# Performance work log

Hardware: AMD Instinct MI355X
Metric: run time of the kernel (lower is better)

Reference implementation:

```python
import jax, jax.numpy as jnp
import numpy as np

B, S, DIM, H, C = 1, 1024, 4096, 32, 8
HD = DIM // H  # 128
NEG = -1e9


def setup_inputs() -> dict:
    key = jax.random.key(0)
    ks = jax.random.split(key, 8)
    scale = 0.02
    x = jax.random.normal(ks[0], (B, S, DIM), jnp.float32)
    wq = jax.random.normal(ks[1], (DIM, DIM), jnp.float32) * scale
    wk = jax.random.normal(ks[2], (DIM, DIM), jnp.float32) * scale
    wv = jax.random.normal(ks[3], (DIM, DIM), jnp.float32) * scale
    wo = jax.random.normal(ks[4], (DIM, DIM), jnp.float32) * scale
    # RoPE tables (theta=10000), matching precompute_freqs_cis
    inv = 1.0 / (10000.0 ** (np.arange(0, HD, 2, dtype=np.float32) / HD))  # [HD/2]
    ang = np.arange(S, dtype=np.float32)[:, None] * inv[None, :]  # [S, HD/2]
    freqs_cos = jnp.asarray(np.cos(ang))
    freqs_sin = jnp.asarray(np.sin(ang))
    # causal mask used at prefill (start_pos == 0)
    mask = jnp.where(jnp.triu(jnp.ones((S, S), bool), k=1), jnp.float32(NEG), 0.0)
    # cluster labels: ensure every cluster non-empty; rep = first head with label
    rng = np.random.default_rng(0)
    lab = np.concatenate([np.arange(C), rng.integers(0, C, H - C)]).astype(np.int32)
    rep = np.array([np.where(lab == c)[0][0] for c in range(C)], dtype=np.int32)
    return {
        "x": x, "wq": wq, "wk": wk, "wv": wv, "wo": wo,
        "freqs_cos": freqs_cos, "freqs_sin": freqs_sin, "mask": mask,
        "cluster_assignment": jnp.asarray(lab), "rep_heads": jnp.asarray(rep),
        "start_pos": 0,
    }


def _rope(x, cos, sin):
    # x: [b, s, h, d]; cos/sin: [s, d/2]; interleaved complex multiply
    xr, xi = x[..., ::2], x[..., 1::2]
    cos = cos[None, :, None, :]
    sin = sin[None, :, None, :]
    orr = xr * cos - xi * sin
    oi = xr * sin + xi * cos
    return jnp.stack([orr, oi], axis=-1).reshape(x.shape)


def reference(x, wq, wk, wv, wo, freqs_cos, freqs_sin, mask,
              cluster_assignment, rep_heads, start_pos):
    b, s, dim = x.shape
    h, d = H, HD
    xq = (x @ wq.T).reshape(b, s, h, d)
    xk = (x @ wk.T).reshape(b, s, h, d)
    xv = (x @ wv.T).reshape(b, s, h, d)
    xq = _rope(xq, freqs_cos, freqs_sin)
    xk = _rope(xk, freqs_cos, freqs_sin)
    xqh = jnp.transpose(xq, (0, 2, 1, 3))  # [b, h, s, d]
    xkh = jnp.transpose(xk, (0, 2, 1, 3))
    vh = jnp.transpose(xv, (0, 2, 1, 3))
    # CHAI: gather representative head per cluster, score once per cluster
    xq_new = xqh[:, rep_heads]  # [b, C, s, d]
    xk_new = xkh[:, rep_heads]
    sc = jnp.einsum("bcqd,bckd->bcqk", xq_new, xk_new) / jnp.sqrt(jnp.float32(d))
    # scatter cluster scores back to every member head (pure gather by label)
    scores = sc[:, cluster_assignment]  # [b, h, s, s]
    scores = scores + mask[None, None]
    p = jax.nn.softmax(scores.astype(jnp.float32), axis=-1).astype(x.dtype)
    out = jnp.einsum("bhqk,bhkd->bhqd", p, vh)
    out = jnp.transpose(out, (0, 2, 1, 3)).reshape(b, s, h * d)
    return out @ wo.T
```

## Files before the change

kernel.cpp:

```cpp
#include <hip/hip_runtime.h>

typedef __bf16 bf16x8 __attribute__((ext_vector_type(8)));
typedef float f32x4 __attribute__((ext_vector_type(4)));
typedef unsigned short u16x8 __attribute__((ext_vector_type(8)));

#define BM 128
#define BN 128
#define BK 64

__device__ __forceinline__ unsigned short f2bf(float f) {
    union { float f; unsigned int u; } x; x.f = f;
    unsigned int u = x.u;
    u += 0x7fffu + ((u >> 16) & 1u);
    return (unsigned short)(u >> 16);
}

__device__ __forceinline__ float bf2f(unsigned short h) {
    union { unsigned int u; float f; } x; x.u = ((unsigned int)h) << 16;
    return x.f;
}

__device__ __forceinline__ void async_copy16(const void* g, void* l) {
    __builtin_amdgcn_global_load_lds(
        (const __attribute__((address_space(1))) void*)(uintptr_t)g,
        (__attribute__((address_space(3))) void*)(uintptr_t)l, 16, 0, 0);
}

__global__ void cvt_all(const float* __restrict__ x, const float* __restrict__ wq,
                        const float* __restrict__ wk, const float* __restrict__ wv,
                        const float* __restrict__ wo, const int* __restrict__ rep,
                        unsigned short* __restrict__ xb, unsigned short* __restrict__ wqkvb,
                        unsigned short* __restrict__ wob) {
    long i = (long)blockIdx.x * 256 + threadIdx.x;
    const float* src;
    unsigned short* dst;
    if (i < 524288) {
        src = x + i * 8;
        dst = xb + i * 8;
    } else if (i < 3670016) {
        long j = i - 524288;
        int r = (int)(j >> 9), c8 = (int)(j & 511);
        const float* s;
        if (r < 1024)      s = wq + ((long)(rep[r >> 7] * 128 + (r & 127)) << 12);
        else if (r < 2048) s = wk + ((long)(rep[(r - 1024) >> 7] * 128 + (r & 127)) << 12);
        else               s = wv + ((long)(r - 2048) << 12);
        src = s + c8 * 8;
        dst = wqkvb + ((long)r << 12) + c8 * 8;
    } else {
        long j = i - 3670016;
        src = wo + j * 8;
        dst = wob + j * 8;
    }
    float4 v0 = ((const float4*)src)[0];
    float4 v1 = ((const float4*)src)[1];
    u16x8 o = { f2bf(v0.x), f2bf(v0.y), f2bf(v0.z), f2bf(v0.w),
                f2bf(v1.x), f2bf(v1.y), f2bf(v1.z), f2bf(v1.w) };
    *(u16x8*)dst = o;
}


template<bool F32OUT, int MODE>
__global__ __launch_bounds__(256, 2) void gemm_bt(
    const unsigned short* __restrict__ A, const unsigned short* __restrict__ B,
    void* __restrict__ Cv, int K, int lda, int ldb, int ldc,
    long long aZ, long long bZ, long long cZ, const int* __restrict__ aIdx,
    int kOffZ, int nby) {
    __shared__ unsigned short As[BM * BK];
    __shared__ unsigned short Bs[BN * BK];

    int L = blockIdx.x;
    int q8 = gridDim.x >> 3;
    int wk_ = (L & 7) * q8 + (L >> 3);
    int bmi = wk_ & 7;
    int t2 = wk_ >> 3;
    int bni = t2 % nby;
    int z = t2 / nby;

    if (MODE == 1 && bni > bmi) return;

    A += (aIdx ? (long long)aIdx[z] : (long long)z) * aZ;
    B += (long long)z * bZ;
    int bm = bmi * BM;
    int bn = bni * BN;
    int t = threadIdx.x;
    int lane = t & 63;
    int w = t >> 6;
    int wr = (w >> 1) * 64, wc = (w & 1) * 64;

    int kt0 = z * kOffZ;
    int kEnd = kt0 + K;
    if (MODE == 2) kEnd = kt0 + min(K, bm + BM);

    f32x4 acc[4][4] = {};

    for (int kt = kt0; kt < kEnd; kt += BK) {
#pragma unroll
        for (int i = 0; i < 4; ++i) {
            int f = i * 256 + t;
            int row = f >> 3;
            int c8 = f & 7;
            async_copy16(A + (long)(bm + row) * lda + kt + c8 * 8, &As[f * 8]);
            async_copy16(B + (long)(bn + row) * ldb + kt + c8 * 8, &Bs[f * 8]);
        }
        asm volatile("s_waitcnt vmcnt(0)" ::: "memory");
        __syncthreads();
#pragma unroll
        for (int kk = 0; kk < BK; kk += 32) {
            bf16x8 a[4], b[4];
            int r0 = lane & 15;
            int kof = kk + ((lane >> 4) << 3);
#pragma unroll
            for (int m = 0; m < 4; ++m)
                a[m] = *(const bf16x8*)&As[(wr + m * 16 + r0) * BK + kof];
#pragma unroll
            for (int n = 0; n < 4; ++n)
                b[n] = *(const bf16x8*)&Bs[(wc + n * 16 + r0) * BK + kof];
#pragma unroll
            for (int m = 0; m < 4; ++m)
#pragma unroll
                for (int n = 0; n < 4; ++n)
                    acc[m][n] = __builtin_amdgcn_mfma_f32_16x16x32_bf16(a[m], b[n], acc[m][n], 0, 0, 0);
        }
        __syncthreads();
    }

    int cl = lane & 15;
    int rbase = (lane >> 4) << 2;
    if (F32OUT) {
        float* C = (float*)Cv + (long long)z * cZ;
#pragma unroll
        for (int m = 0; m < 4; ++m)
#pragma unroll
            for (int n = 0; n < 4; ++n)
#pragma unroll
                for (int j = 0; j < 4; ++j)
                    C[(long)(bm + wr + m * 16 + rbase + j) * ldc + (bn + wc + n * 16 + cl)] = acc[m][n][j];
    } else {
        unsigned short* C = (unsigned short*)Cv + (long long)z * cZ;
#pragma unroll
        for (int m = 0; m < 4; ++m)
#pragma unroll
            for (int n = 0; n < 4; ++n)
#pragma unroll
                for (int j = 0; j < 4; ++j)
                    C[(long)(bm + wr + m * 16 + rbase + j) * ldc + (bn + wc + n * 16 + cl)] = f2bf(acc[m][n][j]);
    }
}

__global__ void reduce_rope(unsigned short* __restrict__ qkv,
                            const float* __restrict__ fc, const float* __restrict__ fs,
                            int nsplit) {
    int s = blockIdx.y;
    int cc = (blockIdx.x * 256 + threadIdx.x) * 8;
    long base = (long)s * 6144 + cc;
    ushort4 a0 = *(const ushort4*)(qkv + base);
    ushort4 a1 = *(const ushort4*)(qkv + base + 4);
    float f[8] = { bf2f(a0.x), bf2f(a0.y), bf2f(a0.z), bf2f(a0.w),
                   bf2f(a1.x), bf2f(a1.y), bf2f(a1.z), bf2f(a1.w) };
    for (int z = 1; z < nsplit; ++z) {
        const unsigned short* p = qkv + (long)z * 6291456;
        ushort4 b0 = *(const ushort4*)(p + base);
        ushort4 b1 = *(const ushort4*)(p + base + 4);
        f[0] += bf2f(b0.x); f[1] += bf2f(b0.y); f[2] += bf2f(b0.z); f[3] += bf2f(b0.w);
        f[4] += bf2f(b1.x); f[5] += bf2f(b1.y); f[6] += bf2f(b1.z); f[7] += bf2f(b1.w);
    }
    if (cc < 2048) {
        int i0 = (cc & 127) >> 1;
        const float* cp = fc + (s << 6) + i0;
        const float* sp = fs + (s << 6) + i0;
#pragma unroll
        for (int p = 0; p < 4; ++p) {
            float co = cp[p], sn = sp[p];
            float x0 = f[2 * p], x1 = f[2 * p + 1];
            f[2 * p] = x0 * co - x1 * sn;
            f[2 * p + 1] = x0 * sn + x1 * co;
        }
    }
    ushort4 o0 = { f2bf(f[0]), f2bf(f[1]), f2bf(f[2]), f2bf(f[3]) };
    ushort4 o1 = { f2bf(f[4]), f2bf(f[5]), f2bf(f[6]), f2bf(f[7]) };
    *(ushort4*)(qkv + base) = o0;
    *(ushort4*)(qkv + base + 4) = o1;
}

__global__ void reduce_out4(const unsigned short* __restrict__ p, float* __restrict__ out) {
    long i = (long)blockIdx.x * 256 + threadIdx.x;
    ushort4 a = ((const ushort4*)p)[i];
    ushort4 b = ((const ushort4*)(p + 4194304))[i];
    ushort4 c = ((const ushort4*)(p + 8388608))[i];
    ushort4 d = ((const ushort4*)(p + 12582912))[i];
    float4 o;
    o.x = bf2f(a.x) + bf2f(b.x) + bf2f(c.x) + bf2f(d.x);
    o.y = bf2f(a.y) + bf2f(b.y) + bf2f(c.y) + bf2f(d.y);
    o.z = bf2f(a.z) + bf2f(b.z) + bf2f(c.z) + bf2f(d.z);
    o.w = bf2f(a.w) + bf2f(b.w) + bf2f(c.w) + bf2f(d.w);
    ((float4*)out)[i] = o;
}

__global__ void transpose_v(const unsigned short* __restrict__ qkv, unsigned short* __restrict__ vt) {
    __shared__ unsigned short tile[32][33];
    int h = blockIdx.z, d0 = blockIdx.x * 32, s0 = blockIdx.y * 32;
    int tx = threadIdx.x & 31, ty = threadIdx.x >> 5;
#pragma unroll
    for (int i = 0; i < 32; i += 8)
        tile[ty + i][tx] = qkv[(long)(s0 + ty + i) * 6144 + 2048 + h * 128 + d0 + tx];
    __syncthreads();
#pragma unroll
    for (int i = 0; i < 32; i += 8)
        vt[(long)h * 131072 + (long)(d0 + ty + i) * 1024 + s0 + tx] = tile[tx][ty + i];
}

__global__ __launch_bounds__(256) void softmax_causal(const unsigned short* __restrict__ sc,
                                                      unsigned short* __restrict__ P) {
    int i = blockIdx.x;
    int c = blockIdx.y;
    long base = ((long)c << 20) + ((long)i << 10);
    const unsigned short* row = sc + base;
    unsigned short* prow = P + base;
    int t = threadIdx.x;
    const float alpha = 0.08838834764831845f;
    int nj = i >> 8;

    float v[4];
    float mx = -3.4e38f;
    for (int j0 = 0; j0 <= nj; ++j0) {
        int j = j0 * 256 + t;
        float x = bf2f(row[j]) * alpha;
        v[j0] = (j <= i) ? x : -3.4e38f;
        mx = fmaxf(mx, v[j0]);
    }
#pragma unroll
    for (int o = 32; o > 0; o >>= 1) mx = fmaxf(mx, __shfl_xor(mx, o));
    __shared__ float red[4];
    int w = t >> 6, lane = t & 63;
    if (lane == 0) red[w] = mx;
    __syncthreads();
    mx = fmaxf(fmaxf(red[0], red[1]), fmaxf(red[2], red[3]));

    float e[4];
    float sum = 0.f;
    for (int j0 = 0; j0 <= nj; ++j0) {
        e[j0] = (v[j0] > -1e37f) ? __expf(v[j0] - mx) : 0.f;
        sum += e[j0];
    }
#pragma unroll
    for (int o = 32; o > 0; o >>= 1) sum += __shfl_xor(sum, o);
    __syncthreads();
    if (lane == 0) red[w] = sum;
    __syncthreads();
    sum = red[0] + red[1] + red[2] + red[3];
    float inv = 1.f / sum;
    for (int j0 = 0; j0 <= nj; ++j0) {
        int j = j0 * 256 + t;
        prow[j] = f2bf(e[j0] * inv);
    }
}


extern "C" void kernel_launch(void* const* d_in, const int* in_sizes, int n_in,
                              void* d_out, int out_size, void* d_ws, size_t ws_size,
                              hipStream_t stream) {
    const float* x  = (const float*)d_in[0];
    const float* wq = (const float*)d_in[1];
    const float* wk = (const float*)d_in[2];
    const float* wv = (const float*)d_in[3];
    const float* wo = (const float*)d_in[4];
    const float* fc = (const float*)d_in[5];
    const float* fs = (const float*)d_in[6];
    const int* lab = (const int*)d_in[8];
    const int* rep = (const int*)d_in[9];
    float* out = (float*)d_out;

    char* ws = (char*)d_ws;
    unsigned short* xb    = (unsigned short*)(ws);
    unsigned short* wqkvb = (unsigned short*)(ws + 8388608);
    unsigned short* wob   = (unsigned short*)(ws + 58720256);
    unsigned short* qkv_s = (unsigned short*)(ws + 92274688);
    unsigned short* vt    = (unsigned short*)(ws + 104857600);
    unsigned short* scores= (unsigned short*)(ws + 8388608);
    unsigned short* P     = (unsigned short*)(ws + 41943040);
    unsigned short* opart = (unsigned short*)(ws + 8388608);
    unsigned short* attn  = xb;

    int skQ = (ws_size >= (size_t)117440512) ? 2 : 1;

    cvt_all<<<22528, 256, 0, stream>>>(x, wq, wk, wv, wo, rep, xb, wqkvb, wob);

    if (skQ == 2) {
        gemm_bt<false, 0><<<768, 256, 0, stream>>>(
            xb, wqkvb, qkv_s, 2048, 4096, 4096, 6144, 0, 0, 6291456, nullptr, 2048, 48);
    } else {
        gemm_bt<false, 0><<<384, 256, 0, stream>>>(
            xb, wqkvb, qkv_s, 4096, 4096, 4096, 6144, 0, 0, 0, nullptr, 0, 48);
    }

    reduce_rope<<<dim3(3, 1024), 256, 0, stream>>>(qkv_s, fc, fs, skQ);
    transpose_v<<<dim3(4, 32, 32), 256, 0, stream>>>(qkv_s, vt);

    gemm_bt<false, 1><<<512, 256, 0, stream>>>(
        qkv_s, qkv_s + 1024, scores, 128, 6144, 6144, 1024,
        128, 128, 1048576, nullptr, 0, 8);

    softmax_causal<<<dim3(1024, 8), 256, 0, stream>>>(scores, P);

    gemm_bt<false, 2><<<256, 256, 0, stream>>>(
        P, vt, attn, 1024, 1024, 1024, 4096,
        1048576, 131072, 128, lab, 0, 1);

    gemm_bt<false, 0><<<1024, 256, 0, stream>>>(
        attn, wob, opart, 1024, 4096, 4096, 4096, 0, 0, 4194304, nullptr, 1024, 32);
    reduce_out4<<<4096, 256, 0, stream>>>(opart, out);
}
```

Measured before the change: 218.2 us.

## Fuse fp32 weight conversion into GEMM loads and swizzle LDS tiles

Removes the separate pass that converted all four fp32 weight matrices to bf16. The QKV and output-projection GEMMs now stream fp32 weights straight into LDS, convert them to bf16 in registers before the MFMA, and apply the representative-head gather inside the kernel. All GEMMs also gain an XOR-swizzled LDS layout to cut bank conflicts. The trade is twice the weight bytes per tile and a larger LDS footprint (fp32 B tile), which may lower occupancy.

New measurement: 211.3 us. 1.03x faster.

```diff
diff --git a/kernel.cpp b/kernel.cpp
--- a/kernel.cpp
+++ b/kernel.cpp
@@ -26,45 +26,118 @@
         (__attribute__((address_space(3))) void*)(uintptr_t)l, 16, 0, 0);
 }
 
-__global__ void cvt_all(const float* __restrict__ x, const float* __restrict__ wq,
-                        const float* __restrict__ wk, const float* __restrict__ wv,
-                        const float* __restrict__ wo, const int* __restrict__ rep,
-                        unsigned short* __restrict__ xb, unsigned short* __restrict__ wqkvb,
-                        unsigned short* __restrict__ wob) {
+__global__ void cvt_x(const float* __restrict__ x, unsigned short* __restrict__ xb) {
     long i = (long)blockIdx.x * 256 + threadIdx.x;
-    const float* src;
-    unsigned short* dst;
-    if (i < 524288) {
-        src = x + i * 8;
-        dst = xb + i * 8;
-    } else if (i < 3670016) {
-        long j = i - 524288;
-        int r = (int)(j >> 9), c8 = (int)(j & 511);
-        const float* s;
-        if (r < 1024)      s = wq + ((long)(rep[r >> 7] * 128 + (r & 127)) << 12);
-        else if (r < 2048) s = wk + ((long)(rep[(r - 1024) >> 7] * 128 + (r & 127)) << 12);
-        else               s = wv + ((long)(r - 2048) << 12);
-        src = s + c8 * 8;
-        dst = wqkvb + ((long)r << 12) + c8 * 8;
-    } else {
-        long j = i - 3670016;
-        src = wo + j * 8;
-        dst = wob + j * 8;
-    }
+    const float* src = x + i * 8;
     float4 v0 = ((const float4*)src)[0];
     float4 v1 = ((const float4*)src)[1];
     u16x8 o = { f2bf(v0.x), f2bf(v0.y), f2bf(v0.z), f2bf(v0.w),
                 f2bf(v1.x), f2bf(v1.y), f2bf(v1.z), f2bf(v1.w) };
-    *(u16x8*)dst = o;
-}
-
-
-template<bool F32OUT, int MODE>
+    *(u16x8*)(xb + i * 8) = o;
+}
+
+template<int GATHER>
+__global__ __launch_bounds__(256, 2) void gemm_wf32(
+    const unsigned short* __restrict__ A, const float* __restrict__ w0,
+    const float* __restrict__ w1, const float* __restrict__ w2,
+    const int* __restrict__ rep, unsigned short* __restrict__ C,
+    int K, int lda, int ldc, long long cZ, int kOffZ, int nby) {
+    __shared__ unsigned short As[BM * BK];
+    __shared__ float BsF[BN * BK];
+
+    int L = blockIdx.x;
+    int q8 = gridDim.x >> 3;
+    int wk_ = (L & 7) * q8 + (L >> 3);
+    int bmi = wk_ & 7;
+    int t2 = wk_ >> 3;
+    int bni = t2 % nby;
+    int z = t2 / nby;
+
+    const float* Bsrc;
+    if (GATHER) {
+        if (bni < 8)       Bsrc = w0 + (long)rep[bni] * 524288;
+        else if (bni < 16) Bsrc = w1 + (long)rep[bni - 8] * 524288;
+        else               Bsrc = w2 + (long)(bni - 16) * 524288;
+    } else {
+        Bsrc = w0 + (long)bni * 524288;
+    }
+
+    int bm = bmi * BM;
+    int t = threadIdx.x;
+    int lane = t & 63;
+    int w = t >> 6;
+    int wr = (w >> 1) * 64, wc = (w & 1) * 64;
+
+    int kt0 = z * kOffZ;
+    int kEnd = kt0 + K;
+
+    f32x4 acc[4][4] = {};
+
+    for (int kt = kt0; kt < kEnd; kt += BK) {
+#pragma unroll
+        for (int i = 0; i < 4; ++i) {
+            int f = i * 256 + t;
+            int row = f >> 3, c8 = f & 7;
+            int cs = c8 ^ (row & 7);
+            async_copy16(A + (long)(bm + row) * lda + kt + cs * 8, &As[f * 8]);
+        }
+#pragma unroll
+        for (int i = 0; i < 8; ++i) {
+            int f = i * 256 + t;
+            int row = f >> 4, c16 = f & 15;
+            int pair = c16 >> 1, w2b = c16 & 1;
+            int ps = pair ^ (row & 7);
+            async_copy16(Bsrc + (long)row * 4096 + kt + ps * 8 + w2b * 4, &BsF[f * 4]);
+        }
+        asm volatile("s_waitcnt vmcnt(0)" ::: "memory");
+        __syncthreads();
+#pragma unroll
+        for (int kk = 0; kk < BK; kk += 32) {
+            bf16x8 a[4], b[4];
+            int r0 = lane & 15;
+            int kof = kk + ((lane >> 4) << 3);
+            int kc = kof >> 3;
+#pragma unroll
+            for (int m = 0; m < 4; ++m) {
+                int ra = wr + m * 16 + r0;
+                a[m] = *(const bf16x8*)&As[ra * 64 + ((kc ^ (ra & 7)) << 3)];
+            }
+#pragma unroll
+            for (int n = 0; n < 4; ++n) {
+                int rb = wc + n * 16 + r0;
+                const f32x4* pb = (const f32x4*)&BsF[rb * 64 + ((kc ^ (rb & 7)) << 3)];
+                f32x4 lo = pb[0], hi = pb[1];
+                bf16x8 bb = { (__bf16)lo[0], (__bf16)lo[1], (__bf16)lo[2], (__bf16)lo[3],
+                              (__bf16)hi[0], (__bf16)hi[1], (__bf16)hi[2], (__bf16)hi[3] };
+                b[n] = bb;
+            }
+#pragma unroll
+            for (int m = 0; m < 4; ++m)
+#pragma unroll
+                for (int n = 0; n < 4; ++n)
+                    acc[m][n] = __builtin_amdgcn_mfma_f32_16x16x32_bf16(a[m], b[n], acc[m][n], 0, 0, 0);
+        }
+        __syncthreads();
+    }
+
+    int cl = lane & 15;
+    int rbase = (lane >> 4) << 2;
+    unsigned short* Cp = C + (long long)z * cZ;
+#pragma unroll
+    for (int m = 0; m < 4; ++m)
+#pragma unroll
+        for (int n = 0; n < 4; ++n)
+#pragma unroll
+            for (int j = 0; j < 4; ++j)
+                Cp[(long)(bm + wr + m * 16 + rbase + j) * ldc + (bni * BN + wc + n * 16 + cl)] = f2bf(acc[m][n][j]);
+}
+
+template<int MODE>
 __global__ __launch_bounds__(256, 2) void gemm_bt(
     const unsigned short* __restrict__ A, const unsigned short* __restrict__ B,
-    void* __restrict__ Cv, int K, int lda, int ldb, int ldc,
+    unsigned short* __restrict__ C, int K, int lda, int ldb, int ldc,
     long long aZ, long long bZ, long long cZ, const int* __restrict__ aIdx,
-    int kOffZ, int nby) {
+    int nby) {
     __shared__ unsigned short As[BM * BK];
     __shared__ unsigned short Bs[BN * BK];
 
@@ -87,20 +160,18 @@
     int w = t >> 6;
     int wr = (w >> 1) * 64, wc = (w & 1) * 64;
 
-    int kt0 = z * kOffZ;
-    int kEnd = kt0 + K;
-    if (MODE == 2) kEnd = kt0 + min(K, bm + BM);
+    int kEnd = (MODE == 2) ? min(K, bm + BM) : K;
 
     f32x4 acc[4][4] = {};
 
-    for (int kt = kt0; kt < kEnd; kt += BK) {
+    for (int kt = 0; kt < kEnd; kt += BK) {
 #pragma unroll
         for (int i = 0; i < 4; ++i) {
             int f = i * 256 + t;
-            int row = f >> 3;
-            int c8 = f & 7;
-            async_copy16(A + (long)(bm + row) * lda + kt + c8 * 8, &As[f * 8]);
-            async_copy16(B + (long)(bn + row) * ldb + kt + c8 * 8, &Bs[f * 8]);
+            int row = f >> 3, c8 = f & 7;
+            int cs = c8 ^ (row & 7);
+            async_copy16(A + (long)(bm + row) * lda + kt + cs * 8, &As[f * 8]);
+            async_copy16(B + (long)(bn + row) * ldb + kt + cs * 8, &Bs[f * 8]);
         }
         asm volatile("s_waitcnt vmcnt(0)" ::: "memory");
         __syncthreads();
@@ -109,12 +180,17 @@
             bf16x8 a[4], b[4];
             int r0 = lane & 15;
             int kof = kk + ((lane >> 4) << 3);
-#pragma unroll
-            for (int m = 0; m < 4; ++m)
-                a[m] = *(const bf16x8*)&As[(wr + m * 16 + r0) * BK + kof];
-#pragma unroll
-            for (int n = 0; n < 4; ++n)
-                b[n] = *(const bf16x8*)&Bs[(wc + n * 16 + r0) * BK + kof];
+            int kc = kof >> 3;
+#pragma unroll
+            for (int m = 0; m < 4; ++m) {
+                int ra = wr + m * 16 + r0;
+                a[m] = *(const bf16x8*)&As[ra * 64 + ((kc ^ (ra & 7)) << 3)];
+            }
+#pragma unroll
+            for (int n = 0; n < 4; ++n) {
+                int rb = wc + n * 16 + r0;
+                b[n] = *(const bf16x8*)&Bs[rb * 64 + ((kc ^ (rb & 7)) << 3)];
+            }
 #pragma unroll
             for (int m = 0; m < 4; ++m)
 #pragma unroll
@@ -126,25 +202,14 @@
 
     int cl = lane & 15;
     int rbase = (lane >> 4) << 2;
-    if (F32OUT) {
-        float* C = (float*)Cv + (long long)z * cZ;
-#pragma unroll
-        for (int m = 0; m < 4; ++m)
-#pragma unroll
-            for (int n = 0; n < 4; ++n)
-#pragma unroll
-                for (int j = 0; j < 4; ++j)
-                    C[(long)(bm + wr + m * 16 + rbase + j) * ldc + (bn + wc + n * 16 + cl)] = acc[m][n][j];
-    } else {
-        unsigned short* C = (unsigned short*)Cv + (long long)z * cZ;
-#pragma unroll
-        for (int m = 0; m < 4; ++m)
-#pragma unroll
-            for (int n = 0; n < 4; ++n)
-#pragma unroll
-                for (int j = 0; j < 4; ++j)
-                    C[(long)(bm + wr + m * 16 + rbase + j) * ldc + (bn + wc + n * 16 + cl)] = f2bf(acc[m][n][j]);
-    }
+    unsigned short* Cp = C + (long long)z * cZ;
+#pragma unroll
+    for (int m = 0; m < 4; ++m)
+#pragma unroll
+        for (int n = 0; n < 4; ++n)
+#pragma unroll
+            for (int j = 0; j < 4; ++j)
+                Cp[(long)(bm + wr + m * 16 + rbase + j) * ldc + (bn + wc + n * 16 + cl)] = f2bf(acc[m][n][j]);
 }
 
 __global__ void reduce_rope(unsigned short* __restrict__ qkv,
@@ -272,41 +337,39 @@
 
     char* ws = (char*)d_ws;
     unsigned short* xb    = (unsigned short*)(ws);
-    unsigned short* wqkvb = (unsigned short*)(ws + 8388608);
-    unsigned short* wob   = (unsigned short*)(ws + 58720256);
-    unsigned short* qkv_s = (unsigned short*)(ws + 92274688);
-    unsigned short* vt    = (unsigned short*)(ws + 104857600);
     unsigned short* scores= (unsigned short*)(ws + 8388608);
     unsigned short* P     = (unsigned short*)(ws + 41943040);
     unsigned short* opart = (unsigned short*)(ws + 8388608);
+    unsigned short* qkv_s = (unsigned short*)(ws + 92274688);
+    unsigned short* vt    = (unsigned short*)(ws + 104857600);
     unsigned short* attn  = xb;
 
     int skQ = (ws_size >= (size_t)117440512) ? 2 : 1;
 
-    cvt_all<<<22528, 256, 0, stream>>>(x, wq, wk, wv, wo, rep, xb, wqkvb, wob);
+    cvt_x<<<2048, 256, 0, stream>>>(x, xb);
 
     if (skQ == 2) {
-        gemm_bt<false, 0><<<768, 256, 0, stream>>>(
-            xb, wqkvb, qkv_s, 2048, 4096, 4096, 6144, 0, 0, 6291456, nullptr, 2048, 48);
+        gemm_wf32<1><<<768, 256, 0, stream>>>(
+            xb, wq, wk, wv, rep, qkv_s, 2048, 4096, 6144, 6291456, 2048, 48);
     } else {
-        gemm_bt<false, 0><<<384, 256, 0, stream>>>(
-            xb, wqkvb, qkv_s, 4096, 4096, 4096, 6144, 0, 0, 0, nullptr, 0, 48);
+        gemm_wf32<1><<<384, 256, 0, stream>>>(
+            xb, wq, wk, wv, rep, qkv_s, 4096, 4096, 6144, 0, 0, 48);
     }
 
     reduce_rope<<<dim3(3, 1024), 256, 0, stream>>>(qkv_s, fc, fs, skQ);
     transpose_v<<<dim3(4, 32, 32), 256, 0, stream>>>(qkv_s, vt);
 
-    gemm_bt<false, 1><<<512, 256, 0, stream>>>(
+    gemm_bt<1><<<512, 256, 0, stream>>>(
         qkv_s, qkv_s + 1024, scores, 128, 6144, 6144, 1024,
-        128, 128, 1048576, nullptr, 0, 8);
+        128, 128, 1048576, nullptr, 8);
 
     softmax_causal<<<dim3(1024, 8), 256, 0, stream>>>(scores, P);
 
-    gemm_bt<false, 2><<<256, 256, 0, stream>>>(
+    gemm_bt<2><<<256, 256, 0, stream>>>(
         P, vt, attn, 1024, 1024, 1024, 4096,
-        1048576, 131072, 128, lab, 0, 1);
-
-    gemm_bt<false, 0><<<1024, 256, 0, stream>>>(
-        attn, wob, opart, 1024, 4096, 4096, 4096, 0, 0, 4194304, nullptr, 1024, 32);
+        1048576, 131072, 128, lab, 1);
+
+    gemm_wf32<0><<<1024, 256, 0, stream>>>(
+        attn, wo, nullptr, nullptr, nullptr, opart, 1024, 4096, 4096, 4194304, 1024, 32);
     reduce_out4<<<4096, 256, 0, stream>>>(opart, out);
 }
```

## Double-buffer LDS tiles and XOR-swizzle columns in bf16 GEMM kernel

Applied to the files above, without the earlier changes.

The shared GEMM kernel now keeps two LDS buffers per operand, so the async global-to-LDS copy of the next K tile is issued before the MFMA work on the current tile. The global wait and barrier move to the end of each iteration. The 16-byte chunk index within each 128-byte LDS row is XOR-swizzled by the row index on both store and load, to cut bank conflicts on the row-strided fragment reads. The unused float-output template path is dropped. LDS per block doubles to 64KB, which may limit occupancy under the two-blocks-per-CU launch bound.

Result: faster. 203.9 us (-6.6%).

```diff
diff --git a/kernel.cpp b/kernel.cpp
--- a/kernel.cpp
+++ b/kernel.cpp
@@ -58,15 +58,14 @@
     *(u16x8*)dst = o;
 }
 
-
-template<bool F32OUT, int MODE>
+template<int MODE>
 __global__ __launch_bounds__(256, 2) void gemm_bt(
     const unsigned short* __restrict__ A, const unsigned short* __restrict__ B,
-    void* __restrict__ Cv, int K, int lda, int ldb, int ldc,
+    unsigned short* __restrict__ C, int K, int lda, int ldb, int ldc,
     long long aZ, long long bZ, long long cZ, const int* __restrict__ aIdx,
     int kOffZ, int nby) {
-    __shared__ unsigned short As[BM * BK];
-    __shared__ unsigned short Bs[BN * BK];
+    __shared__ unsigned short As[2][BM * BK];
+    __shared__ unsigned short Bs[2][BN * BK];
 
     int L = blockIdx.x;
     int q8 = gridDim.x >> 3;
@@ -87,64 +86,69 @@
     int w = t >> 6;
     int wr = (w >> 1) * 64, wc = (w & 1) * 64;
 
-    int kt0 = z * kOffZ;
-    int kEnd = kt0 + K;
-    if (MODE == 2) kEnd = kt0 + min(K, bm + BM);
+    int kt0 = (MODE == 0) ? z * kOffZ : 0;
+    int kEnd = kt0 + ((MODE == 2) ? min(K, bm + BM) : K);
+
+#define STAGE(buf, kt) \
+    _Pragma("unroll") \
+    for (int i = 0; i < 4; ++i) { \
+        int f = i * 256 + t; \
+        int row = f >> 3, c8 = f & 7; \
+        int cs = c8 ^ (row & 7); \
+        async_copy16(A + (long)(bm + row) * lda + (kt) + cs * 8, &As[buf][f * 8]); \
+        async_copy16(B + (long)(bn + row) * ldb + (kt) + cs * 8, &Bs[buf][f * 8]); \
+    }
 
     f32x4 acc[4][4] = {};
 
+    STAGE(0, kt0);
+    asm volatile("s_waitcnt vmcnt(0)" ::: "memory");
+    __syncthreads();
+
+    int cur = 0;
     for (int kt = kt0; kt < kEnd; kt += BK) {
-#pragma unroll
-        for (int i = 0; i < 4; ++i) {
-            int f = i * 256 + t;
-            int row = f >> 3;
-            int c8 = f & 7;
-            async_copy16(A + (long)(bm + row) * lda + kt + c8 * 8, &As[f * 8]);
-            async_copy16(B + (long)(bn + row) * ldb + kt + c8 * 8, &Bs[f * 8]);
-        }
-        asm volatile("s_waitcnt vmcnt(0)" ::: "memory");
-        __syncthreads();
+        if (kt + BK < kEnd) { STAGE(cur ^ 1, kt + BK); }
+
+        const unsigned short* Asc = As[cur];
+        const unsigned short* Bsc = Bs[cur];
 #pragma unroll
         for (int kk = 0; kk < BK; kk += 32) {
             bf16x8 a[4], b[4];
             int r0 = lane & 15;
             int kof = kk + ((lane >> 4) << 3);
-#pragma unroll
-            for (int m = 0; m < 4; ++m)
-                a[m] = *(const bf16x8*)&As[(wr + m * 16 + r0) * BK + kof];
-#pragma unroll
-            for (int n = 0; n < 4; ++n)
-                b[n] = *(const bf16x8*)&Bs[(wc + n * 16 + r0) * BK + kof];
+            int kc = kof >> 3;
+#pragma unroll
+            for (int m = 0; m < 4; ++m) {
+                int ra = wr + m * 16 + r0;
+                a[m] = *(const bf16x8*)&Asc[ra * 64 + ((kc ^ (ra & 7)) << 3)];
+            }
+#pragma unroll
+            for (int n = 0; n < 4; ++n) {
+                int rb = wc + n * 16 + r0;
+                b[n] = *(const bf16x8*)&Bsc[rb * 64 + ((kc ^ (rb & 7)) << 3)];
+            }
 #pragma unroll
             for (int m = 0; m < 4; ++m)
 #pragma unroll
                 for (int n = 0; n < 4; ++n)
                     acc[m][n] = __builtin_amdgcn_mfma_f32_16x16x32_bf16(a[m], b[n], acc[m][n], 0, 0, 0);
         }
+        asm volatile("s_waitcnt vmcnt(0)" ::: "memory");
         __syncthreads();
-    }
+        cur ^= 1;
+    }
+#undef STAGE
 
     int cl = lane & 15;
     int rbase = (lane >> 4) << 2;
-    if (F32OUT) {
-        float* C = (float*)Cv + (long long)z * cZ;
-#pragma unroll
-        for (int m = 0; m < 4; ++m)
-#pragma unroll
-            for (int n = 0; n < 4; ++n)
-#pragma unroll
-                for (int j = 0; j < 4; ++j)
-                    C[(long)(bm + wr + m * 16 + rbase + j) * ldc + (bn + wc + n * 16 + cl)] = acc[m][n][j];
-    } else {
-        unsigned short* C = (unsigned short*)Cv + (long long)z * cZ;
-#pragma unroll
-        for (int m = 0; m < 4; ++m)
-#pragma unroll
-            for (int n = 0; n < 4; ++n)
-#pragma unroll
-                for (int j = 0; j < 4; ++j)
-                    C[(long)(bm + wr + m * 16 + rbase + j) * ldc + (bn + wc + n * 16 + cl)] = f2bf(acc[m][n][j]);
-    }
+    unsigned short* Cp = C + (long long)z * cZ;
+#pragma unroll
+    for (int m = 0; m < 4; ++m)
+#pragma unroll
+        for (int n = 0; n < 4; ++n)
+#pragma unroll
+            for (int j = 0; j < 4; ++j)
+                Cp[(long)(bm + wr + m * 16 + rbase + j) * ldc + (bn + wc + n * 16 + cl)] = f2bf(acc[m][n][j]);
 }
 
 __global__ void reduce_rope(unsigned short* __restrict__ qkv,
@@ -286,27 +290,27 @@
     cvt_all<<<22528, 256, 0, stream>>>(x, wq, wk, wv, wo, rep, xb, wqkvb, wob);
 
     if (skQ == 2) {
-        gemm_bt<false, 0><<<768, 256, 0, stream>>>(
+        gemm_bt<0><<<768, 256, 0, stream>>>(
             xb, wqkvb, qkv_s, 2048, 4096, 4096, 6144, 0, 0, 6291456, nullptr, 2048, 48);
     } else {
-        gemm_bt<false, 0><<<384, 256, 0, stream>>>(
+        gemm_bt<0><<<384, 256, 0, stream>>>(
             xb, wqkvb, qkv_s, 4096, 4096, 4096, 6144, 0, 0, 0, nullptr, 0, 48);
     }
 
     reduce_rope<<<dim3(3, 1024), 256, 0, stream>>>(qkv_s, fc, fs, skQ);
     transpose_v<<<dim3(4, 32, 32), 256, 0, stream>>>(qkv_s, vt);
 
-    gemm_bt<false, 1><<<512, 256, 0, stream>>>(
+    gemm_bt<1><<<512, 256, 0, stream>>>(
         qkv_s, qkv_s + 1024, scores, 128, 6144, 6144, 1024,
         128, 128, 1048576, nullptr, 0, 8);
 
     softmax_causal<<<dim3(1024, 8), 256, 0, stream>>>(scores, P);
 
-    gemm_bt<false, 2><<<256, 256, 0, stream>>>(
+    gemm_bt<2><<<256, 256, 0, stream>>>(
         P, vt, attn, 1024, 1024, 1024, 4096,
         1048576, 131072, 128, lab, 0, 1);
 
-    gemm_bt<false, 0><<<1024, 256, 0, stream>>>(
+    gemm_bt<0><<<1024, 256, 0, stream>>>(
         attn, wob, opart, 1024, 4096, 4096, 4096, 0, 0, 4194304, nullptr, 1024, 32);
     reduce_out4<<<4096, 256, 0, stream>>>(opart, out);
 }
```
